# Kernel optimization log

Hardware: AMD Instinct MI355X
Metric: run time of the kernel (lower is better)

## Reference

```python
import jax, jax.numpy as jnp
import numpy as np

N_NODES = 100000
N_EDGES = 1600000
N_OBS = 48
HIDDEN = 48
N_ACT = 32


def setup_inputs() -> dict:
    key = jax.random.key(0)
    ks = jax.random.split(key, 6)
    x = jax.random.normal(ks[0], (N_OBS, N_NODES), dtype=jnp.float32)
    onehot = jax.random.uniform(ks[1], (1, N_NODES), dtype=jnp.float32)
    W1 = jax.random.normal(ks[2], (N_OBS, HIDDEN), dtype=jnp.float32) * (1.0 / np.sqrt(N_OBS))
    b1 = jnp.zeros((HIDDEN,), dtype=jnp.float32)
    W2 = jax.random.normal(ks[3], (HIDDEN, N_ACT), dtype=jnp.float32) * (1.0 / np.sqrt(HIDDEN))
    b2 = jnp.zeros((N_ACT,), dtype=jnp.float32)
    edge_index = jax.random.randint(ks[4], (2, N_EDGES), 0, N_NODES, dtype=jnp.int64)
    return {"x": x, "onehot": onehot, "W1": W1, "b1": b1, "W2": W2, "b2": b2, "edge_index": edge_index}


def reference(x, onehot, W1, b1, W2, b2, edge_index):
    # graph.x is stored transposed; forward does x = graph.x.T -> [N, F]
    h = x.T  # [N, n_obs]
    n = h.shape[0]
    # GCNConv default: add self-loops, symmetric deg^-1/2 normalization
    loops = jnp.arange(n, dtype=edge_index.dtype)
    row = jnp.concatenate([edge_index[0], loops])  # source nodes
    col = jnp.concatenate([edge_index[1], loops])  # target nodes
    deg = jax.ops.segment_sum(jnp.ones(row.shape, dtype=h.dtype), col, num_segments=n)
    dinv = jnp.where(deg > 0, jax.lax.rsqrt(jnp.maximum(deg, 1.0)), 0.0)
    norm = dinv[row] * dinv[col]  # [E+N]

    def conv(feat, W, b):
        feat = feat @ W                         # tiny dense GEMM [N, d_out]
        msg = norm[:, None] * feat[row]         # gather + scale  [E+N, d_out]
        return jax.ops.segment_sum(msg, col, num_segments=n) + b  # scatter-add

    # dropout is identity in eval mode
    h = jax.nn.relu(conv(h, W1, b1))
    h = conv(h, W2, b2)                          # [N, n_actions]
    return onehot @ h                            # [1, n_actions]
```

## Files before the change

kernel.cpp:

```cpp
#include <hip/hip_runtime.h>

#define CAP 64
#define NBUCK 512
#define NPB 196
#define NPH 98
#define GCAPH 1792
#define LCAP 24
#define GCAP 3584
#define NBIN 256
#define QAMAX0 6.0f
#define QS0 (127.0f / QAMAX0)
#define QAMAX1 4.0f
#define INVQS1 (QAMAX1 / 127.0f)
#define SMEM1 53248

__device__ __forceinline__ void bin_pass(const int* __restrict__ pay,
                                         const int* __restrict__ key, int E,
                                         int* __restrict__ bcur,
                                         unsigned* __restrict__ barr,
                                         char* smem, int binBlk) {
    unsigned* buf = (unsigned*)smem;
    int* cnt  = (int*)(buf + NBUCK * LCAP);
    int* base = cnt + NBUCK;
    for (int i = threadIdx.x; i < NBUCK; i += 256) cnt[i] = 0;
    __syncthreads();
    int epb = (E + NBIN - 1) / NBIN;
    int start = binBlk * epb;
    int end = min(E, start + epb);
    for (int e0 = start + threadIdx.x; e0 < end; e0 += 256 * 4) {
        int rr[4], cc[4];
#pragma unroll
        for (int k = 0; k < 4; k++) {
            int e = e0 + k * 256;
            if (e < end) { rr[k] = pay[e]; cc[k] = key[e]; }
        }
#pragma unroll
        for (int k = 0; k < 4; k++) {
            int e = e0 + k * 256;
            if (e < end) {
                int b = cc[k] / NPB;
                unsigned ent = ((unsigned)rr[k] << 8) | (unsigned)(cc[k] - b * NPB);
                int p = atomicAdd(&cnt[b], 1);
                if (p < LCAP) buf[b * LCAP + p] = ent;
                else {
                    int gp = atomicAdd(&bcur[b], 1);
                    if (gp < GCAP) barr[(size_t)b * GCAP + gp] = ent;
                }
            }
        }
    }
    __syncthreads();
    for (int b = threadIdx.x; b < NBUCK; b += 256)
        base[b] = atomicAdd(&bcur[b], min(cnt[b], LCAP));
    __syncthreads();
    for (int idx = threadIdx.x; idx < NBUCK * LCAP; idx += 256) {
        int b = idx / LCAP, slot = idx - b * LCAP;
        if (slot < min(cnt[b], LCAP)) {
            int gp = base[b] + slot;
            if (gp < GCAP) barr[(size_t)b * GCAP + gp] = buf[idx];
        }
    }
}

__launch_bounds__(256)
__global__ void k_bin_gemm(const int* __restrict__ row, const int* __restrict__ col,
                           int E, int* __restrict__ bcur1, unsigned* __restrict__ barr1,
                           int* __restrict__ bcur2, unsigned* __restrict__ barr2,
                           const float* __restrict__ x, const float* __restrict__ W1,
                           const float* __restrict__ onehot,
                           unsigned* __restrict__ q0, float* __restrict__ ohsum,
                           float* __restrict__ out, int N) {
    __shared__ __align__(16) char smem[SMEM1];
    if (blockIdx.x < NBIN) {
        bin_pass(row, col, E, bcur1, barr1, smem, blockIdx.x);
    } else if (blockIdx.x < 2 * NBIN) {
        bin_pass(col, row, E, bcur2, barr2, smem, blockIdx.x - NBIN);
    } else {
        if (blockIdx.x == 2 * NBIN && threadIdx.x < 32) out[threadIdx.x] = 0.f;
        float* Ws = (float*)smem;
        float* ohred = Ws + 48 * 48;
        for (int i = threadIdx.x; i < 48 * 48; i += 256) Ws[i] = W1[i];
        __syncthreads();
        int n = (blockIdx.x - 2 * NBIN) * 256 + threadIdx.x;
        float oh = 0.f;
        if (n < N) {
            float acc[48];
#pragma unroll
            for (int j = 0; j < 48; j++) acc[j] = 0.f;
#pragma unroll 4
            for (int k = 0; k < 48; k++) {
                float xv = x[(size_t)k * N + n];
#pragma unroll
                for (int j = 0; j < 48; j++) acc[j] += xv * Ws[k * 48 + j];
            }
            oh = onehot[n];
            unsigned* qp = q0 + (size_t)n * 12;
#pragma unroll
            for (int p = 0; p < 12; p++) {
                unsigned u = 0;
#pragma unroll
                for (int k = 0; k < 4; k++) {
                    int b = __float2int_rn(acc[4 * p + k] * QS0);
                    b = (b < -127 ? -127 : (b > 127 ? 127 : b)) + 128;
                    u |= ((unsigned)b) << (8 * k);
                }
                qp[p] = u;
            }
        }
        ohred[threadIdx.x] = oh;
        __syncthreads();
        for (int off = 128; off > 0; off >>= 1) {
            if (threadIdx.x < off) ohred[threadIdx.x] += ohred[threadIdx.x + off];
            __syncthreads();
        }
        if (threadIdx.x == 0) atomicAdd(ohsum, ohred[0]);
    }
}

__launch_bounds__(256)
__global__ void k_build(const unsigned* __restrict__ barr1,
                        const int* __restrict__ bcur1,
                        int* __restrict__ csr, long long* __restrict__ sd,
                        const float* __restrict__ onehot, float* __restrict__ t,
                        const unsigned* __restrict__ q0, unsigned* __restrict__ q,
                        int N) {
    __shared__ int csr_s[GCAPH];
    __shared__ int cnt_s[NPH];
    __shared__ int scan_s[128];
    __shared__ int cur_s[NPH];
    int b = blockIdx.x >> 1, half = blockIdx.x & 1;
    int lnbase = half * NPH;
    for (int i = threadIdx.x; i < NPH; i += 256) cnt_s[i] = 0;
    __syncthreads();
    int bn = min(bcur1[b], GCAP);
    const unsigned* bp = barr1 + (size_t)b * GCAP;
    int nbase = b * NPB + lnbase;
    for (int i = threadIdx.x; i < bn; i += 256) {
        int lnh = (int)(bp[i] & 0xffu) - lnbase;
        if ((unsigned)lnh < NPH) atomicAdd(&cnt_s[lnh], 1);
    }
    __syncthreads();
    int v = (threadIdx.x < NPH) ? cnt_s[threadIdx.x] : 0;
    if (threadIdx.x < 128) scan_s[threadIdx.x] = v;
    __syncthreads();
    for (int off = 1; off < 128; off <<= 1) {
        int tv = (threadIdx.x >= off && threadIdx.x < 128) ? scan_s[threadIdx.x - off] : 0;
        __syncthreads();
        if (threadIdx.x < 128) scan_s[threadIdx.x] += tv;
        __syncthreads();
    }
    if (threadIdx.x < NPH) cur_s[threadIdx.x] = scan_s[threadIdx.x] - v;
    __syncthreads();
    for (int i = threadIdx.x; i < bn; i += 256) {
        unsigned e = bp[i];
        int lnh = (int)(e & 0xffu) - lnbase;
        if ((unsigned)lnh < NPH) {
            int p = atomicAdd(&cur_s[lnh], 1);
            if (p < GCAPH) csr_s[p] = (int)(e >> 8);
        }
    }
    __syncthreads();
    int tot = min(scan_s[NPH - 1], GCAPH);
    int gbase = b * GCAP + half * GCAPH;
    for (int i = threadIdx.x; i < tot; i += 256)
        csr[gbase + i] = csr_s[i];
    for (int i = threadIdx.x; i < NPH; i += 256) {
        int n = nbase + i;
        if (n < N) {
            int d = cnt_s[i];
            long long st = (long long)(gbase + (scan_s[i] - d));
            sd[n] = st | ((long long)d << 32);
            t[n] = onehot[n] * rsqrtf((float)(d + 1));
        }
    }
    for (int idx = threadIdx.x; idx < NPH * 12; idx += 256) {
        int i = idx / 12, p = idx - i * 12;
        int n = nbase + i;
        if (n < N) {
            float r = 1.5f * rsqrtf((float)(cnt_s[i] + 1));
            unsigned u = q0[(size_t)n * 12 + p];
            unsigned o = 0;
#pragma unroll
            for (int k = 0; k < 4; k++) {
                int bq = (int)((u >> (8 * k)) & 0xffu) - 128;
                int nb = __float2int_rn((float)bq * r);
                nb = (nb < -127 ? -127 : (nb > 127 ? 127 : nb)) + 128;
                o |= ((unsigned)nb) << (8 * k);
            }
            q[((size_t)n << 4) + p] = o;
        } else {
            q[((size_t)n << 4) + p] = 0u;
        }
    }
}

__launch_bounds__(256)
__global__ void k_gather_buildw(const unsigned* __restrict__ barr2,
                                const int* __restrict__ bcur2,
                                const float* __restrict__ t, float* __restrict__ w,
                                const int* __restrict__ csr,
                                const long long* __restrict__ sd,
                                const unsigned* __restrict__ q,
                                const float* __restrict__ b1, const float* __restrict__ W2,
                                float* __restrict__ g2, int N) {
    __shared__ float W2s[48 * 32];
    __shared__ float a1s[16][48];
    const unsigned M = 0x00FF00FFu;
    if (blockIdx.x < NBUCK) {
        float* wacc = (float*)W2s;
        int b = blockIdx.x;
        for (int i = threadIdx.x; i < NPB; i += 256) wacc[i] = 0.f;
        __syncthreads();
        int bn = min(bcur2[b], GCAP);
        const unsigned* bp = barr2 + (size_t)b * GCAP;
        int nbase = b * NPB;
        for (int i = threadIdx.x; i < bn; i += 256) {
            unsigned e = __builtin_nontemporal_load(&bp[i]);
            atomicAdd(&wacc[e & 0xffu], t[e >> 8]);
        }
        __syncthreads();
        for (int i = threadIdx.x; i < NPB; i += 256) {
            int n = nbase + i;
            if (n < N) w[n] = wacc[i] + t[n];
        }
        return;
    }
    for (int i = threadIdx.x; i < 48 * 32; i += 256) W2s[i] = W2[i];
    int wv = threadIdx.x >> 6, lane = threadIdx.x & 63;
    int quarter = lane >> 4, lane16 = lane & 15;
    int s = lane16 >> 2, j = lane16 & 3;
    int node = wv * 4 + quarter;
    int c = (blockIdx.x - NBUCK) * 16 + node;
    float dv = 0.f;
    if (c < N) {
        long long sdv = __builtin_nontemporal_load(&sd[c]);
        int beg = (int)(sdv & 0xffffffffLL), dg = (int)(sdv >> 32);
        int dd = dg < CAP ? dg : CAP;
        dv = rsqrtf((float)(dg + 1));
        int idx[4];
#pragma unroll
        for (int k = 0; k < 4; k++)
            idx[k] = (16 * k + lane16 < dd)
                         ? __builtin_nontemporal_load(&csr[beg + 16 * k + lane16]) : 0;
        unsigned aE0 = 0, aO0 = 0, aE1 = 0, aO1 = 0;
        unsigned aE2 = 0, aO2 = 0, aE3 = 0, aO3 = 0;
        if (s == 0) {
            uint4 v0 = *((const uint4*)(q + ((size_t)c << 4)) + j);
            aE0 = v0.x & M; aO0 = (v0.x >> 8) & M;
            aE1 = v0.y & M; aO1 = (v0.y >> 8) & M;
            aE2 = v0.z & M; aO2 = (v0.z >> 8) & M;
            aE3 = v0.w & M; aO3 = (v0.w >> 8) & M;
        }
        uint4 st[16];
#pragma unroll
        for (int g = 0; g < 16; g++) {
            if (4 * g < dd) {
                int e = 4 * g + s;
                int src = __shfl(idx[g >> 2], quarter * 16 + (e & 15));
                src = (e < dd) ? src : N;
                st[g] = *((const uint4*)(q + ((size_t)src << 4)) + j);
            }
        }
        __builtin_amdgcn_sched_barrier(0);
#pragma unroll
        for (int g = 0; g < 16; g++) {
            if (4 * g < dd) {
                aE0 += st[g].x & M; aO0 += (st[g].x >> 8) & M;
                aE1 += st[g].y & M; aO1 += (st[g].y >> 8) & M;
                aE2 += st[g].z & M; aO2 += (st[g].z >> 8) & M;
                aE3 += st[g].w & M; aO3 += (st[g].w >> 8) & M;
            }
        }
#pragma unroll
        for (int off = 8; off >= 4; off >>= 1) {
            aE0 += (unsigned)__shfl_down((int)aE0, off, 16);
            aO0 += (unsigned)__shfl_down((int)aO0, off, 16);
            aE1 += (unsigned)__shfl_down((int)aE1, off, 16);
            aO1 += (unsigned)__shfl_down((int)aO1, off, 16);
            aE2 += (unsigned)__shfl_down((int)aE2, off, 16);
            aO2 += (unsigned)__shfl_down((int)aO2, off, 16);
            aE3 += (unsigned)__shfl_down((int)aE3, off, 16);
            aO3 += (unsigned)__shfl_down((int)aO3, off, 16);
        }
        if (s == 0 && j < 3) {
            float cnt = (float)(dd + 1);
            float gsc = dv * INVQS1;
            float corr = 128.f * cnt;
            const float4* b4 = (const float4*)b1;
            float4* as4 = (float4*)a1s[node];
            float S0, S1, S2, S3;
            float4 o;
            S0 = (float)(aE0 & 0xffffu); S1 = (float)(aO0 & 0xffffu);
            S2 = (float)(aE0 >> 16);     S3 = (float)(aO0 >> 16);
            float4 bw = b4[4 * j + 0];
            o.x = fmaxf(gsc * (S0 - corr) + bw.x, 0.f);
            o.y = fmaxf(gsc * (S1 - corr) + bw.y, 0.f);
            o.z = fmaxf(gsc * (S2 - corr) + bw.z, 0.f);
            o.w = fmaxf(gsc * (S3 - corr) + bw.w, 0.f);
            as4[4 * j + 0] = o;
            S0 = (float)(aE1 & 0xffffu); S1 = (float)(aO1 & 0xffffu);
            S2 = (float)(aE1 >> 16);     S3 = (float)(aO1 >> 16);
            bw = b4[4 * j + 1];
            o.x = fmaxf(gsc * (S0 - corr) + bw.x, 0.f);
            o.y = fmaxf(gsc * (S1 - corr) + bw.y, 0.f);
            o.z = fmaxf(gsc * (S2 - corr) + bw.z, 0.f);
            o.w = fmaxf(gsc * (S3 - corr) + bw.w, 0.f);
            as4[4 * j + 1] = o;
            S0 = (float)(aE2 & 0xffffu); S1 = (float)(aO2 & 0xffffu);
            S2 = (float)(aE2 >> 16);     S3 = (float)(aO2 >> 16);
            bw = b4[4 * j + 2];
            o.x = fmaxf(gsc * (S0 - corr) + bw.x, 0.f);
            o.y = fmaxf(gsc * (S1 - corr) + bw.y, 0.f);
            o.z = fmaxf(gsc * (S2 - corr) + bw.z, 0.f);
            o.w = fmaxf(gsc * (S3 - corr) + bw.w, 0.f);
            as4[4 * j + 2] = o;
            S0 = (float)(aE3 & 0xffffu); S1 = (float)(aO3 & 0xffffu);
            S2 = (float)(aE3 >> 16);     S3 = (float)(aO3 >> 16);
            bw = b4[4 * j + 3];
            o.x = fmaxf(gsc * (S0 - corr) + bw.x, 0.f);
            o.y = fmaxf(gsc * (S1 - corr) + bw.y, 0.f);
            o.z = fmaxf(gsc * (S2 - corr) + bw.z, 0.f);
            o.w = fmaxf(gsc * (S3 - corr) + bw.w, 0.f);
            as4[4 * j + 3] = o;
        }
    }
    __syncthreads();
    if (c < N) {
        int f0 = lane16 * 2;
        float a = 0.f, b = 0.f;
#pragma unroll
        for (int k = 0; k < 48; k++) {
            float av = a1s[node][k];
            a += av * W2s[k * 32 + f0];
            b += av * W2s[k * 32 + f0 + 1];
        }
        __builtin_nontemporal_store(dv * a, &g2[(size_t)c * 32 + f0]);
        __builtin_nontemporal_store(dv * b, &g2[(size_t)c * 32 + f0 + 1]);
    }
}

__global__ void k_final3(const float* __restrict__ g2, const float* __restrict__ w,
                         const float* __restrict__ ohsum, const float* __restrict__ b2,
                         float* __restrict__ out, int N) {
    __shared__ float s[256];
    int tid = threadIdx.x;
    int total = N * 32;
    int stride = gridDim.x * 256;
    float acc = 0.f;
    for (int i = blockIdx.x * 256 + tid; i < total; i += stride)
        acc += w[i >> 5] * g2[i];
    s[tid] = acc;
    __syncthreads();
    for (int off = 128; off >= 32; off >>= 1) {
        if (tid < off) s[tid] += s[tid + off];
        __syncthreads();
    }
    if (tid < 32) {
        float v = s[tid];
        if (blockIdx.x == 0) v += b2[tid] * ohsum[0];
        atomicAdd(&out[tid], v);
    }
}

extern "C" void kernel_launch(void* const* d_in, const int* in_sizes, int n_in,
                              void* d_out, int out_size, void* d_ws, size_t ws_size,
                              hipStream_t stream) {
    const float* x      = (const float*)d_in[0];
    const float* onehot = (const float*)d_in[1];
    const float* W1     = (const float*)d_in[2];
    const float* b1     = (const float*)d_in[3];
    const float* W2     = (const float*)d_in[4];
    const float* b2     = (const float*)d_in[5];
    const int*   ei     = (const int*)d_in[6];

    int N = in_sizes[1];
    int E = in_sizes[6] / 2;
    const int* row = ei;
    const int* col = ei + E;

    char* wsb = (char*)d_ws;
    int*       bcur1  = (int*)wsb;          wsb += NBUCK * 4;
    int*       bcur2  = (int*)wsb;          wsb += NBUCK * 4;
    float*     ohsum  = (float*)wsb;        wsb += 32;
    unsigned*  barr1  = (unsigned*)wsb;     wsb += (size_t)NBUCK * GCAP * 4;
    unsigned*  barr2  = (unsigned*)wsb;     wsb += (size_t)NBUCK * GCAP * 4;
    int*       csr    = (int*)wsb;          wsb += (size_t)NBUCK * GCAP * 4;
    long long* sd     = (long long*)wsb;    wsb += (size_t)N * 8;
    float*     t      = (float*)wsb;        wsb += (size_t)N * 4;
    float*     w      = (float*)wsb;        wsb += (size_t)N * 4;
    unsigned*  q      = (unsigned*)wsb;     wsb += ((size_t)NBUCK * NPB + 1) * 16 * 4;
    unsigned*  q0     = (unsigned*)wsb;
    float*     g2     = (float*)wsb;        wsb += (size_t)N * 32 * 4;

    hipMemsetAsync(bcur1, 0, NBUCK * 4 * 2 + 32, stream);

    int nGB = (N + 255) / 256;
    int NB = (N + 15) / 16;
    k_bin_gemm<<<2 * NBIN + nGB, 256, 0, stream>>>(row, col, E, bcur1, barr1,
                                                   bcur2, barr2, x, W1, onehot,
                                                   q0, ohsum, (float*)d_out, N);
    k_build<<<2 * NBUCK, 256, 0, stream>>>(barr1, bcur1, csr, sd,
                                           onehot, t, q0, q, N);
    k_gather_buildw<<<NBUCK + NB, 256, 0, stream>>>(barr2, bcur2, t, w,
                                                    csr, sd, q,
                                                    b1, W2, g2, N);
    k_final3<<<256, 256, 0, stream>>>(g2, w, ohsum, b2, (float*)d_out, N);
}
```

Measured before the change: 200.6 us.

## Fuse CSR build, gather, w-accumulation and final reduction into one kernel

The pipeline is restructured. k_build now only computes t and the rescaled q. A new fused kernel rebuilds each half-bucket's CSR in shared memory, accumulates the w weights, runs the layer-1 gather and the layer-2 GEMV, and folds the onehot-weighted reduction into per-block atomics on the output. This removes the global csr/sd/w/g2 round trips and the separate final-reduction launch. In exchange, each block now runs the count/scan work alongside the gather (the first count pass is done twice, once in k_tq and again in the fused kernel), and it has only 1024 blocks looping 7 passes with extra barriers, which may cost parallelism and latency hiding.

```diff
diff --git a/kernel.cpp b/kernel.cpp
--- a/kernel.cpp
+++ b/kernel.cpp
@@ -118,62 +118,26 @@
 }
 
 __launch_bounds__(256)
-__global__ void k_build(const unsigned* __restrict__ barr1,
-                        const int* __restrict__ bcur1,
-                        int* __restrict__ csr, long long* __restrict__ sd,
-                        const float* __restrict__ onehot, float* __restrict__ t,
-                        const unsigned* __restrict__ q0, unsigned* __restrict__ q,
-                        int N) {
-    __shared__ int csr_s[GCAPH];
-    __shared__ int cnt_s[NPH];
-    __shared__ int scan_s[128];
-    __shared__ int cur_s[NPH];
-    int b = blockIdx.x >> 1, half = blockIdx.x & 1;
-    int lnbase = half * NPH;
-    for (int i = threadIdx.x; i < NPH; i += 256) cnt_s[i] = 0;
+__global__ void k_tq(const unsigned* __restrict__ barr1,
+                     const int* __restrict__ bcur1,
+                     const float* __restrict__ onehot, float* __restrict__ t,
+                     const unsigned* __restrict__ q0, unsigned* __restrict__ q,
+                     int N) {
+    __shared__ int cnt_s[NPB];
+    int b = blockIdx.x;
+    for (int i = threadIdx.x; i < NPB; i += 256) cnt_s[i] = 0;
     __syncthreads();
     int bn = min(bcur1[b], GCAP);
     const unsigned* bp = barr1 + (size_t)b * GCAP;
-    int nbase = b * NPB + lnbase;
-    for (int i = threadIdx.x; i < bn; i += 256) {
-        int lnh = (int)(bp[i] & 0xffu) - lnbase;
-        if ((unsigned)lnh < NPH) atomicAdd(&cnt_s[lnh], 1);
-    }
-    __syncthreads();
-    int v = (threadIdx.x < NPH) ? cnt_s[threadIdx.x] : 0;
-    if (threadIdx.x < 128) scan_s[threadIdx.x] = v;
-    __syncthreads();
-    for (int off = 1; off < 128; off <<= 1) {
-        int tv = (threadIdx.x >= off && threadIdx.x < 128) ? scan_s[threadIdx.x - off] : 0;
-        __syncthreads();
-        if (threadIdx.x < 128) scan_s[threadIdx.x] += tv;
-        __syncthreads();
-    }
-    if (threadIdx.x < NPH) cur_s[threadIdx.x] = scan_s[threadIdx.x] - v;
-    __syncthreads();
-    for (int i = threadIdx.x; i < bn; i += 256) {
-        unsigned e = bp[i];
-        int lnh = (int)(e & 0xffu) - lnbase;
-        if ((unsigned)lnh < NPH) {
-            int p = atomicAdd(&cur_s[lnh], 1);
-            if (p < GCAPH) csr_s[p] = (int)(e >> 8);
-        }
-    }
-    __syncthreads();
-    int tot = min(scan_s[NPH - 1], GCAPH);
-    int gbase = b * GCAP + half * GCAPH;
-    for (int i = threadIdx.x; i < tot; i += 256)
-        csr[gbase + i] = csr_s[i];
-    for (int i = threadIdx.x; i < NPH; i += 256) {
+    for (int i = threadIdx.x; i < bn; i += 256)
+        atomicAdd(&cnt_s[bp[i] & 0xffu], 1);
+    __syncthreads();
+    int nbase = b * NPB;
+    for (int i = threadIdx.x; i < NPB; i += 256) {
         int n = nbase + i;
-        if (n < N) {
-            int d = cnt_s[i];
-            long long st = (long long)(gbase + (scan_s[i] - d));
-            sd[n] = st | ((long long)d << 32);
-            t[n] = onehot[n] * rsqrtf((float)(d + 1));
-        }
-    }
-    for (int idx = threadIdx.x; idx < NPH * 12; idx += 256) {
+        if (n < N) t[n] = onehot[n] * rsqrtf((float)(cnt_s[i] + 1));
+    }
+    for (int idx = threadIdx.x; idx < NPB * 12; idx += 256) {
         int i = idx / 12, p = idx - i * 12;
         int n = nbase + i;
         if (n < N) {
@@ -195,170 +159,202 @@
 }
 
 __launch_bounds__(256)
-__global__ void k_gather_buildw(const unsigned* __restrict__ barr2,
-                                const int* __restrict__ bcur2,
-                                const float* __restrict__ t, float* __restrict__ w,
-                                const int* __restrict__ csr,
-                                const long long* __restrict__ sd,
-                                const unsigned* __restrict__ q,
-                                const float* __restrict__ b1, const float* __restrict__ W2,
-                                float* __restrict__ g2, int N) {
+__global__ void k_fused3(const unsigned* __restrict__ barr1,
+                         const int* __restrict__ bcur1,
+                         const unsigned* __restrict__ barr2,
+                         const int* __restrict__ bcur2,
+                         const float* __restrict__ t,
+                         const unsigned* __restrict__ q,
+                         const float* __restrict__ b1, const float* __restrict__ W2,
+                         const float* __restrict__ b2, const float* __restrict__ ohsum,
+                         float* __restrict__ out, int N) {
+    __shared__ int csr_s[GCAPH];
+    __shared__ int cnt_s[NPH];
+    __shared__ int scan_s[128];
+    __shared__ int cur_s[NPH];
     __shared__ float W2s[48 * 32];
     __shared__ float a1s[16][48];
+    __shared__ float wacc_s[NPH];
     const unsigned M = 0x00FF00FFu;
-    if (blockIdx.x < NBUCK) {
-        float* wacc = (float*)W2s;
-        int b = blockIdx.x;
-        for (int i = threadIdx.x; i < NPB; i += 256) wacc[i] = 0.f;
-        __syncthreads();
-        int bn = min(bcur2[b], GCAP);
-        const unsigned* bp = barr2 + (size_t)b * GCAP;
-        int nbase = b * NPB;
-        for (int i = threadIdx.x; i < bn; i += 256) {
-            unsigned e = __builtin_nontemporal_load(&bp[i]);
-            atomicAdd(&wacc[e & 0xffu], t[e >> 8]);
-        }
-        __syncthreads();
-        for (int i = threadIdx.x; i < NPB; i += 256) {
-            int n = nbase + i;
-            if (n < N) w[n] = wacc[i] + t[n];
-        }
-        return;
-    }
-    for (int i = threadIdx.x; i < 48 * 32; i += 256) W2s[i] = W2[i];
-    int wv = threadIdx.x >> 6, lane = threadIdx.x & 63;
+    int tid = threadIdx.x;
+    int b = blockIdx.x >> 1, half = blockIdx.x & 1;
+    int lnbase = half * NPH;
+    int nbase = b * NPB + lnbase;
+
+    for (int i = tid; i < NPH; i += 256) cnt_s[i] = 0;
+    __syncthreads();
+    int bn = min(bcur1[b], GCAP);
+    const unsigned* bp = barr1 + (size_t)b * GCAP;
+    for (int i = tid; i < bn; i += 256) {
+        int lnh = (int)(bp[i] & 0xffu) - lnbase;
+        if ((unsigned)lnh < NPH) atomicAdd(&cnt_s[lnh], 1);
+    }
+    __syncthreads();
+    int v = (tid < NPH) ? cnt_s[tid] : 0;
+    if (tid < 128) scan_s[tid] = v;
+    __syncthreads();
+    for (int off = 1; off < 128; off <<= 1) {
+        int tv = (tid >= off && tid < 128) ? scan_s[tid - off] : 0;
+        __syncthreads();
+        if (tid < 128) scan_s[tid] += tv;
+        __syncthreads();
+    }
+    if (tid < NPH) cur_s[tid] = scan_s[tid] - v;
+    __syncthreads();
+    for (int i = tid; i < bn; i += 256) {
+        unsigned e = bp[i];
+        int lnh = (int)(e & 0xffu) - lnbase;
+        if ((unsigned)lnh < NPH) {
+            int p = atomicAdd(&cur_s[lnh], 1);
+            if (p < GCAPH) csr_s[p] = (int)(e >> 8);
+        }
+    }
+    for (int i = tid; i < 48 * 32; i += 256) W2s[i] = W2[i];
+    __syncthreads();
+
+    for (int i = tid; i < NPH; i += 256) wacc_s[i] = 0.f;
+    __syncthreads();
+    int bn2 = min(bcur2[b], GCAP);
+    const unsigned* bp2 = barr2 + (size_t)b * GCAP;
+    for (int i = tid; i < bn2; i += 256) {
+        unsigned e = __builtin_nontemporal_load(&bp2[i]);
+        int lnh = (int)(e & 0xffu) - lnbase;
+        if ((unsigned)lnh < NPH) atomicAdd(&wacc_s[lnh], t[e >> 8]);
+    }
+    __syncthreads();
+    for (int i = tid; i < NPH; i += 256) {
+        int n = nbase + i;
+        if (n < N) wacc_s[i] += t[n];
+    }
+    __syncthreads();
+
+    int wv = tid >> 6, lane = tid & 63;
     int quarter = lane >> 4, lane16 = lane & 15;
     int s = lane16 >> 2, j = lane16 & 3;
     int node = wv * 4 + quarter;
-    int c = (blockIdx.x - NBUCK) * 16 + node;
-    float dv = 0.f;
-    if (c < N) {
-        long long sdv = __builtin_nontemporal_load(&sd[c]);
-        int beg = (int)(sdv & 0xffffffffLL), dg = (int)(sdv >> 32);
-        int dd = dg < CAP ? dg : CAP;
-        dv = rsqrtf((float)(dg + 1));
-        int idx[4];
-#pragma unroll
-        for (int k = 0; k < 4; k++)
-            idx[k] = (16 * k + lane16 < dd)
-                         ? __builtin_nontemporal_load(&csr[beg + 16 * k + lane16]) : 0;
-        unsigned aE0 = 0, aO0 = 0, aE1 = 0, aO1 = 0;
-        unsigned aE2 = 0, aO2 = 0, aE3 = 0, aO3 = 0;
-        if (s == 0) {
-            uint4 v0 = *((const uint4*)(q + ((size_t)c << 4)) + j);
-            aE0 = v0.x & M; aO0 = (v0.x >> 8) & M;
-            aE1 = v0.y & M; aO1 = (v0.y >> 8) & M;
-            aE2 = v0.z & M; aO2 = (v0.z >> 8) & M;
-            aE3 = v0.w & M; aO3 = (v0.w >> 8) & M;
-        }
-        uint4 st[16];
-#pragma unroll
-        for (int g = 0; g < 16; g++) {
-            if (4 * g < dd) {
-                int e = 4 * g + s;
-                int src = __shfl(idx[g >> 2], quarter * 16 + (e & 15));
-                src = (e < dd) ? src : N;
-                st[g] = *((const uint4*)(q + ((size_t)src << 4)) + j);
-            }
-        }
-        __builtin_amdgcn_sched_barrier(0);
-#pragma unroll
-        for (int g = 0; g < 16; g++) {
-            if (4 * g < dd) {
-                aE0 += st[g].x & M; aO0 += (st[g].x >> 8) & M;
-                aE1 += st[g].y & M; aO1 += (st[g].y >> 8) & M;
-                aE2 += st[g].z & M; aO2 += (st[g].z >> 8) & M;
-                aE3 += st[g].w & M; aO3 += (st[g].w >> 8) & M;
-            }
-        }
-#pragma unroll
-        for (int off = 8; off >= 4; off >>= 1) {
-            aE0 += (unsigned)__shfl_down((int)aE0, off, 16);
-            aO0 += (unsigned)__shfl_down((int)aO0, off, 16);
-            aE1 += (unsigned)__shfl_down((int)aE1, off, 16);
-            aO1 += (unsigned)__shfl_down((int)aO1, off, 16);
-            aE2 += (unsigned)__shfl_down((int)aE2, off, 16);
-            aO2 += (unsigned)__shfl_down((int)aO2, off, 16);
-            aE3 += (unsigned)__shfl_down((int)aE3, off, 16);
-            aO3 += (unsigned)__shfl_down((int)aO3, off, 16);
-        }
-        if (s == 0 && j < 3) {
-            float cnt = (float)(dd + 1);
-            float gsc = dv * INVQS1;
-            float corr = 128.f * cnt;
-            const float4* b4 = (const float4*)b1;
-            float4* as4 = (float4*)a1s[node];
-            float S0, S1, S2, S3;
-            float4 o;
-            S0 = (float)(aE0 & 0xffffu); S1 = (float)(aO0 & 0xffffu);
-            S2 = (float)(aE0 >> 16);     S3 = (float)(aO0 >> 16);
-            float4 bw = b4[4 * j + 0];
-            o.x = fmaxf(gsc * (S0 - corr) + bw.x, 0.f);
-            o.y = fmaxf(gsc * (S1 - corr) + bw.y, 0.f);
-            o.z = fmaxf(gsc * (S2 - corr) + bw.z, 0.f);
-            o.w = fmaxf(gsc * (S3 - corr) + bw.w, 0.f);
-            as4[4 * j + 0] = o;
-            S0 = (float)(aE1 & 0xffffu); S1 = (float)(aO1 & 0xffffu);
-            S2 = (float)(aE1 >> 16);     S3 = (float)(aO1 >> 16);
-            bw = b4[4 * j + 1];
-            o.x = fmaxf(gsc * (S0 - corr) + bw.x, 0.f);
-            o.y = fmaxf(gsc * (S1 - corr) + bw.y, 0.f);
-            o.z = fmaxf(gsc * (S2 - corr) + bw.z, 0.f);
-            o.w = fmaxf(gsc * (S3 - corr) + bw.w, 0.f);
-            as4[4 * j + 1] = o;
-            S0 = (float)(aE2 & 0xffffu); S1 = (float)(aO2 & 0xffffu);
-            S2 = (float)(aE2 >> 16);     S3 = (float)(aO2 >> 16);
-            bw = b4[4 * j + 2];
-            o.x = fmaxf(gsc * (S0 - corr) + bw.x, 0.f);
-            o.y = fmaxf(gsc * (S1 - corr) + bw.y, 0.f);
-            o.z = fmaxf(gsc * (S2 - corr) + bw.z, 0.f);
-            o.w = fmaxf(gsc * (S3 - corr) + bw.w, 0.f);
-            as4[4 * j + 2] = o;
-            S0 = (float)(aE3 & 0xffffu); S1 = (float)(aO3 & 0xffffu);
-            S2 = (float)(aE3 >> 16);     S3 = (float)(aO3 >> 16);
-            bw = b4[4 * j + 3];
-            o.x = fmaxf(gsc * (S0 - corr) + bw.x, 0.f);
-            o.y = fmaxf(gsc * (S1 - corr) + bw.y, 0.f);
-            o.z = fmaxf(gsc * (S2 - corr) + bw.z, 0.f);
-            o.w = fmaxf(gsc * (S3 - corr) + bw.w, 0.f);
-            as4[4 * j + 3] = o;
-        }
-    }
-    __syncthreads();
-    if (c < N) {
-        int f0 = lane16 * 2;
-        float a = 0.f, b = 0.f;
-#pragma unroll
-        for (int k = 0; k < 48; k++) {
-            float av = a1s[node][k];
-            a += av * W2s[k * 32 + f0];
-            b += av * W2s[k * 32 + f0 + 1];
-        }
-        __builtin_nontemporal_store(dv * a, &g2[(size_t)c * 32 + f0]);
-        __builtin_nontemporal_store(dv * b, &g2[(size_t)c * 32 + f0 + 1]);
-    }
-}
-
-__global__ void k_final3(const float* __restrict__ g2, const float* __restrict__ w,
-                         const float* __restrict__ ohsum, const float* __restrict__ b2,
-                         float* __restrict__ out, int N) {
-    __shared__ float s[256];
-    int tid = threadIdx.x;
-    int total = N * 32;
-    int stride = gridDim.x * 256;
-    float acc = 0.f;
-    for (int i = blockIdx.x * 256 + tid; i < total; i += stride)
-        acc += w[i >> 5] * g2[i];
-    s[tid] = acc;
-    __syncthreads();
-    for (int off = 128; off >= 32; off >>= 1) {
-        if (tid < off) s[tid] += s[tid + off];
-        __syncthreads();
-    }
+    float accA = 0.f, accB = 0.f;
+    for (int pass = 0; pass < 7; pass++) {
+        int i = pass * 16 + node;
+        int c = nbase + i;
+        bool valid = (i < NPH) && (c < N);
+        float dv = 0.f;
+        if (valid) {
+            int dg = cnt_s[i];
+            int beg = scan_s[i] - dg;
+            int dd = dg < CAP ? dg : CAP;
+            dv = rsqrtf((float)(dg + 1));
+            int idx4[4];
+#pragma unroll
+            for (int k = 0; k < 4; k++)
+                idx4[k] = (16 * k + lane16 < dd) ? csr_s[beg + 16 * k + lane16] : 0;
+            unsigned aE0 = 0, aO0 = 0, aE1 = 0, aO1 = 0;
+            unsigned aE2 = 0, aO2 = 0, aE3 = 0, aO3 = 0;
+            if (s == 0) {
+                uint4 v0 = *((const uint4*)(q + ((size_t)c << 4)) + j);
+                aE0 = v0.x & M; aO0 = (v0.x >> 8) & M;
+                aE1 = v0.y & M; aO1 = (v0.y >> 8) & M;
+                aE2 = v0.z & M; aO2 = (v0.z >> 8) & M;
+                aE3 = v0.w & M; aO3 = (v0.w >> 8) & M;
+            }
+            uint4 st[16];
+#pragma unroll
+            for (int g = 0; g < 16; g++) {
+                if (4 * g < dd) {
+                    int e = 4 * g + s;
+                    int src = __shfl(idx4[g >> 2], quarter * 16 + (e & 15));
+                    src = (e < dd) ? src : N;
+                    st[g] = *((const uint4*)(q + ((size_t)src << 4)) + j);
+                }
+            }
+            __builtin_amdgcn_sched_barrier(0);
+#pragma unroll
+            for (int g = 0; g < 16; g++) {
+                if (4 * g < dd) {
+                    aE0 += st[g].x & M; aO0 += (st[g].x >> 8) & M;
+                    aE1 += st[g].y & M; aO1 += (st[g].y >> 8) & M;
+                    aE2 += st[g].z & M; aO2 += (st[g].z >> 8) & M;
+                    aE3 += st[g].w & M; aO3 += (st[g].w >> 8) & M;
+                }
+            }
+#pragma unroll
+            for (int off = 8; off >= 4; off >>= 1) {
+                aE0 += (unsigned)__shfl_down((int)aE0, off, 16);
+                aO0 += (unsigned)__shfl_down((int)aO0, off, 16);
+                aE1 += (unsigned)__shfl_down((int)aE1, off, 16);
+                aO1 += (unsigned)__shfl_down((int)aO1, off, 16);
+                aE2 += (unsigned)__shfl_down((int)aE2, off, 16);
+                aO2 += (unsigned)__shfl_down((int)aO2, off, 16);
+                aE3 += (unsigned)__shfl_down((int)aE3, off, 16);
+                aO3 += (unsigned)__shfl_down((int)aO3, off, 16);
+            }
+            if (s == 0 && j < 3) {
+                float cnt = (float)(dd + 1);
+                float gsc = dv * INVQS1;
+                float corr = 128.f * cnt;
+                const float4* b4 = (const float4*)b1;
+                float4* as4 = (float4*)a1s[node];
+                float S0, S1, S2, S3;
+                float4 o, bw;
+                S0 = (float)(aE0 & 0xffffu); S1 = (float)(aO0 & 0xffffu);
+                S2 = (float)(aE0 >> 16);     S3 = (float)(aO0 >> 16);
+                bw = b4[4 * j + 0];
+                o.x = fmaxf(gsc * (S0 - corr) + bw.x, 0.f);
+                o.y = fmaxf(gsc * (S1 - corr) + bw.y, 0.f);
+                o.z = fmaxf(gsc * (S2 - corr) + bw.z, 0.f);
+                o.w = fmaxf(gsc * (S3 - corr) + bw.w, 0.f);
+                as4[4 * j + 0] = o;
+                S0 = (float)(aE1 & 0xffffu); S1 = (float)(aO1 & 0xffffu);
+                S2 = (float)(aE1 >> 16);     S3 = (float)(aO1 >> 16);
+                bw = b4[4 * j + 1];
+                o.x = fmaxf(gsc * (S0 - corr) + bw.x, 0.f);
+                o.y = fmaxf(gsc * (S1 - corr) + bw.y, 0.f);
+                o.z = fmaxf(gsc * (S2 - corr) + bw.z, 0.f);
+                o.w = fmaxf(gsc * (S3 - corr) + bw.w, 0.f);
+                as4[4 * j + 1] = o;
+                S0 = (float)(aE2 & 0xffffu); S1 = (float)(aO2 & 0xffffu);
+                S2 = (float)(aE2 >> 16);     S3 = (float)(aO2 >> 16);
+                bw = b4[4 * j + 2];
+                o.x = fmaxf(gsc * (S0 - corr) + bw.x, 0.f);
+                o.y = fmaxf(gsc * (S1 - corr) + bw.y, 0.f);
+                o.z = fmaxf(gsc * (S2 - corr) + bw.z, 0.f);
+                o.w = fmaxf(gsc * (S3 - corr) + bw.w, 0.f);
+                as4[4 * j + 2] = o;
+                S0 = (float)(aE3 & 0xffffu); S1 = (float)(aO3 & 0xffffu);
+                S2 = (float)(aE3 >> 16);     S3 = (float)(aO3 >> 16);
+                bw = b4[4 * j + 3];
+                o.x = fmaxf(gsc * (S0 - corr) + bw.x, 0.f);
+                o.y = fmaxf(gsc * (S1 - corr) + bw.y, 0.f);
+                o.z = fmaxf(gsc * (S2 - corr) + bw.z, 0.f);
+                o.w = fmaxf(gsc * (S3 - corr) + bw.w, 0.f);
+                as4[4 * j + 3] = o;
+            }
+        }
+        __syncthreads();
+        if (valid) {
+            int f0 = lane16 * 2;
+            float a = 0.f, bb = 0.f;
+#pragma unroll
+            for (int k = 0; k < 48; k++) {
+                float av = a1s[node][k];
+                a += av * W2s[k * 32 + f0];
+                bb += av * W2s[k * 32 + f0 + 1];
+            }
+            float wn = wacc_s[i] * dv;
+            accA += wn * a;
+            accB += wn * bb;
+        }
+        __syncthreads();
+    }
+    float* red = &a1s[0][0];
+    red[node * 32 + 2 * lane16]     = accA;
+    red[node * 32 + 2 * lane16 + 1] = accB;
+    __syncthreads();
     if (tid < 32) {
-        float v = s[tid];
-        if (blockIdx.x == 0) v += b2[tid] * ohsum[0];
-        atomicAdd(&out[tid], v);
+        float ssum = 0.f;
+#pragma unroll
+        for (int k = 0; k < 16; k++) ssum += red[k * 32 + tid];
+        if (blockIdx.x == 0) ssum += b2[tid] * ohsum[0];
+        atomicAdd(&out[tid], ssum);
     }
 }
 
@@ -384,25 +380,18 @@
     float*     ohsum  = (float*)wsb;        wsb += 32;
     unsigned*  barr1  = (unsigned*)wsb;     wsb += (size_t)NBUCK * GCAP * 4;
     unsigned*  barr2  = (unsigned*)wsb;     wsb += (size_t)NBUCK * GCAP * 4;
-    int*       csr    = (int*)wsb;          wsb += (size_t)NBUCK * GCAP * 4;
-    long long* sd     = (long long*)wsb;    wsb += (size_t)N * 8;
     float*     t      = (float*)wsb;        wsb += (size_t)N * 4;
-    float*     w      = (float*)wsb;        wsb += (size_t)N * 4;
+    unsigned*  q0     = (unsigned*)wsb;     wsb += (size_t)N * 12 * 4;
     unsigned*  q      = (unsigned*)wsb;     wsb += ((size_t)NBUCK * NPB + 1) * 16 * 4;
-    unsigned*  q0     = (unsigned*)wsb;
-    float*     g2     = (float*)wsb;        wsb += (size_t)N * 32 * 4;
 
     hipMemsetAsync(bcur1, 0, NBUCK * 4 * 2 + 32, stream);
 
     int nGB = (N + 255) / 256;
-    int NB = (N + 15) / 16;
     k_bin_gemm<<<2 * NBIN + nGB, 256, 0, stream>>>(row, col, E, bcur1, barr1,
                                                    bcur2, barr2, x, W1, onehot,
                                                    q0, ohsum, (float*)d_out, N);
-    k_build<<<2 * NBUCK, 256, 0, stream>>>(barr1, bcur1, csr, sd,
-                                           onehot, t, q0, q, N);
-    k_gather_buildw<<<NBUCK + NB, 256, 0, stream>>>(barr2, bcur2, t, w,
-                                                    csr, sd, q,
-                                                    b1, W2, g2, N);
-    k_final3<<<256, 256, 0, stream>>>(g2, w, ohsum, b2, (float*)d_out, N);
-}
+    k_tq<<<NBUCK, 256, 0, stream>>>(barr1, bcur1, onehot, t, q0, q, N);
+    k_fused3<<<2 * NBUCK, 256, 0, stream>>>(barr1, bcur1, barr2, bcur2,
+                                            t, q, b1, W2, b2, ohsum,
+                                            (float*)d_out, N);
+}
```

Result: slower. 222.3 us (+10.8%).
